# Performance work log

Measured on AMD Instinct MI355X. Metric: run time of the kernel, lower is better.

The kernel has to match this reference:

```python
import jax, jax.numpy as jnp
import numpy as np

VOCAB, NUM_CLASSES, E, H = 50257, 20, 64, 64
B, T = 128, 2048


def setup_inputs() -> dict:
    key = jax.random.key(0)
    ks = jax.random.split(key, 16)
    s_ih = 1.0 / np.sqrt(H)
    u = lambda k, shape: jax.random.uniform(k, shape, jnp.float32, -s_ih, s_ih)
    return {
        'tokens': jax.random.randint(ks[0], (B, T), 0, VOCAB),
        'emb': jax.random.normal(ks[1], (VOCAB, E), jnp.float32),
        # forward-direction GRU params (PyTorch layout: [3H, *], gate order r,z,n)
        'wih_f': u(ks[2], (3 * H, E)), 'whh_f': u(ks[3], (3 * H, H)),
        'bih_f': u(ks[4], (3 * H,)), 'bhh_f': u(ks[5], (3 * H,)),
        # backward-direction GRU params
        'wih_b': u(ks[6], (3 * H, E)), 'whh_b': u(ks[7], (3 * H, H)),
        'bih_b': u(ks[8], (3 * H,)), 'bhh_b': u(ks[9], (3 * H,)),
        # classifier: Linear(4H -> H), GELU, Linear(H -> C)
        'w1': u(ks[10], (H, 4 * H)), 'b1': u(ks[11], (H,)),
        'w2': u(ks[12], (NUM_CLASSES, H)), 'b2': u(ks[13], (NUM_CLASSES,)),
    }


def _gru_dir(x, wih, whh, bih, bhh):
    # x: [B, T, E] -> outputs [B, T, H]; PyTorch GRU gate math, gates (r, z, n)
    xg = jnp.einsum('bte,ge->tbg', x, wih) + bih  # precompute input projections [T,B,3H]
    h0 = jnp.zeros((x.shape[0], H), x.dtype)

    def step(h, xg_t):
        hg = h @ whh.T + bhh
        xr, xz, xn = jnp.split(xg_t, 3, axis=-1)
        hr, hz, hn = jnp.split(hg, 3, axis=-1)
        r = jax.nn.sigmoid(xr + hr)
        z = jax.nn.sigmoid(xz + hz)
        n = jnp.tanh(xn + r * hn)
        h_new = (1.0 - z) * n + z * h
        return h_new, h_new

    _, hs = jax.lax.scan(step, h0, xg)  # hs: [T, B, H]
    return hs.transpose(1, 0, 2)


def reference(tokens, emb, wih_f, whh_f, bih_f, bhh_f,
              wih_b, whh_b, bih_b, bhh_b, w1, b1, w2, b2):
    x = emb[tokens]  # [B, T, E]
    h_fwd = _gru_dir(x, wih_f, whh_f, bih_f, bhh_f)
    h_bwd = _gru_dir(x[:, ::-1], wih_b, whh_b, bih_b, bhh_b)[:, ::-1]
    encoded = jnp.concatenate([h_fwd, h_bwd], axis=-1)  # [B, T, 2H]
    feats = jnp.concatenate([encoded.mean(axis=1), encoded.max(axis=1)], axis=-1)  # [B, 4H]
    hid = jax.nn.gelu(feats @ w1.T + b1, approximate=False)
    return hid @ w2.T + b2  # [B, C]
```

## Files before the change

### kernel.cpp

```cpp
#include <hip/hip_runtime.h>
#include <hip/hip_bf16.h>
#include <math.h>

#define VOCAB 50257
#define NCLS 20
#define EDIM 64
#define HDIM 64
#define BATCH 128
#define TLEN 2048

typedef float v2f __attribute__((ext_vector_type(2)));

__device__ float g_P[(size_t)2 * VOCAB * 192];
__device__ float g_feats[BATCH * 256];

__device__ __forceinline__ float fast_rcp(float x) { return __builtin_amdgcn_rcpf(x); }

__device__ __forceinline__ float fsigmoid(float x) {
    return fast_rcp(1.f + __expf(-x));
}
__device__ __forceinline__ float ftanh(float x) {
    float e = __expf(2.f * x);
    return 1.f - 2.f * fast_rcp(e + 1.f);
}

__global__ __launch_bounds__(384) void precompute_P(
    const float* __restrict__ emb,
    const float* __restrict__ wih_f, const float* __restrict__ bih_f,
    const float* __restrict__ wih_b, const float* __restrict__ bih_b)
{
    const int t = threadIdx.x;
    const int dir = t / 192;
    const int g = t % 192;
    const float* wih = dir ? wih_b : wih_f;
    const float* bih = dir ? bih_b : bih_f;

    float4 wq0, wq1, wq2, wq3, wq4, wq5, wq6, wq7;
    float4 wq8, wq9, wq10, wq11, wq12, wq13, wq14, wq15;
#define LDWQ(K) wq##K = *(const float4*)(wih + (size_t)g * 64 + 4 * K)
    LDWQ(0); LDWQ(1); LDWQ(2); LDWQ(3); LDWQ(4); LDWQ(5); LDWQ(6); LDWQ(7);
    LDWQ(8); LDWQ(9); LDWQ(10); LDWQ(11); LDWQ(12); LDWQ(13); LDWQ(14); LDWQ(15);
#undef LDWQ
    const float bias = bih[g];
    float* Pd = g_P + (size_t)dir * VOCAB * 192;

    for (int v = blockIdx.x * 2; v < VOCAB; v += gridDim.x * 2) {
        const int v1ok = (v + 1 < VOCAB);
        const float4* e0 = (const float4*)(emb + (size_t)v * 64);
        const float4* e1 = (const float4*)(emb + (size_t)(v1ok ? v + 1 : v) * 64);
        float a0 = bias, a1 = bias;
#define PFMA(K) do {                                   \
            float4 x = e0[K];                          \
            float4 y = e1[K];                          \
            a0 = fmaf(x.x, wq##K.x, a0);               \
            a1 = fmaf(y.x, wq##K.x, a1);               \
            a0 = fmaf(x.y, wq##K.y, a0);               \
            a1 = fmaf(y.y, wq##K.y, a1);               \
            a0 = fmaf(x.z, wq##K.z, a0);               \
            a1 = fmaf(y.z, wq##K.z, a1);               \
            a0 = fmaf(x.w, wq##K.w, a0);               \
            a1 = fmaf(y.w, wq##K.w, a1);               \
        } while (0)
        PFMA(0); PFMA(1); PFMA(2); PFMA(3); PFMA(4); PFMA(5); PFMA(6); PFMA(7);
        PFMA(8); PFMA(9); PFMA(10); PFMA(11); PFMA(12); PFMA(13); PFMA(14); PFMA(15);
#undef PFMA
        Pd[(size_t)v * 192 + g] = a0;
        if (v1ok) Pd[(size_t)(v + 1) * 192 + g] = a1;
    }
}

__global__ __launch_bounds__(768, 1) void gru_seq(
    const int* __restrict__ tokens,
    const float* __restrict__ whh_f, const float* __restrict__ bhh_f,
    const float* __restrict__ whh_b, const float* __restrict__ bhh_b)
{
    const int tid = threadIdx.x;
    const int gate = tid >> 8;
    const int j = tid & 255;
    const int u = j >> 2;
    const int c = j & 3;
    const int blk = blockIdx.x;
    const int b = blk >> 1;
    const int dir = blk & 1;
    const float* whh = dir ? whh_b : whh_f;
    const float* bhh = dir ? bhh_b : bhh_f;
    const float* Pd = g_P + (size_t)dir * VOCAB * 192 + gate * 64 + u;

    __shared__ __align__(16) float h_lds[64];
    __shared__ float r_lds[64];
    __shared__ float z_lds[64];
    __shared__ __align__(16) int tok_lds[TLEN];

    {
        const int4* src = (const int4*)(tokens + (size_t)b * TLEN);
        int4* dst = (int4*)tok_lds;
        for (int t = tid; t < TLEN / 4; t += 768) dst[t] = src[t];
    }

    v2f w0, w1, w2, w3, w4, w5, w6, w7;
    {
        const float4* p = (const float4*)(whh + (size_t)(gate * 64 + u) * 64 + c * 16);
        float4 q0 = p[0]; w0 = (v2f){q0.x, q0.y}; w1 = (v2f){q0.z, q0.w};
        float4 q1 = p[1]; w2 = (v2f){q1.x, q1.y}; w3 = (v2f){q1.z, q1.w};
        float4 q2 = p[2]; w4 = (v2f){q2.x, q2.y}; w5 = (v2f){q2.z, q2.w};
        float4 q3 = p[3]; w6 = (v2f){q3.x, q3.y}; w7 = (v2f){q3.z, q3.w};
    }
    const float bias = bhh[gate * 64 + u];

    if (tid < 64) h_lds[tid] = 0.f;
    float h = 0.f, sum = 0.f, mx = -INFINITY;
    __syncthreads();

    auto tok_at = [&](int s) -> int {
        int ss = s < TLEN ? s : TLEN - 1;
        return tok_lds[dir ? (TLEN - 1 - ss) : ss];
    };

    float x0, x1, x2, x3;
#define GRU_PRE(SL, D) \
    asm volatile("global_load_dword %0, %1, off" : "=v"(x##SL) : "v"(Pd + (size_t)tok_at(D) * 192))
    GRU_PRE(0, 0); GRU_PRE(1, 1); GRU_PRE(2, 2); GRU_PRE(3, 3);

#define GRU_STEP(SL, SB) do {                                                      \
        const int tN_ = tok_at((SB) + 4);    \
        const float4* hb_ = (const float4*)(h_lds + c * 16);                       \
        v2f a0 = {0.f, 0.f}, a1 = {0.f, 0.f};                                      \
        { float4 h4_ = hb_[0];                                                     \
          a0 = __builtin_elementwise_fma((v2f){h4_.x, h4_.y}, w0, a0);             \
          a1 = __builtin_elementwise_fma((v2f){h4_.z, h4_.w}, w1, a1); }           \
        { float4 h4_ = hb_[1];                                                     \
          a0 = __builtin_elementwise_fma((v2f){h4_.x, h4_.y}, w2, a0);             \
          a1 = __builtin_elementwise_fma((v2f){h4_.z, h4_.w}, w3, a1); }           \
        { float4 h4_ = hb_[2];                                                     \
          a0 = __builtin_elementwise_fma((v2f){h4_.x, h4_.y}, w4, a0);             \
          a1 = __builtin_elementwise_fma((v2f){h4_.z, h4_.w}, w5, a1); }           \
        { float4 h4_ = hb_[3];                                                     \
          a0 = __builtin_elementwise_fma((v2f){h4_.x, h4_.y}, w6, a0);             \
          a1 = __builtin_elementwise_fma((v2f){h4_.z, h4_.w}, w7, a1); }           \
        float p_ = (a0.x + a0.y) + (a1.x + a1.y);                                  \
        float t_ = p_ + __shfl_xor(p_, 1);               \
        float hg = t_ + __shfl_xor(t_, 2);                                         \
        if (gate != 2) {                                                           \
                    \
            asm volatile("s_waitcnt vmcnt(3)" : "+v"(x##SL));                      \
            float g_ = fsigmoid(x##SL + hg + bias);                                \
            if (c == 0) (gate == 0 ? r_lds : z_lds)[u] = g_;                       \
            asm volatile("global_load_dword %0, %1, off"                           \
                         : "=v"(x##SL) : "v"(Pd + (size_t)tN_ * 192));             \
        }                                                                          \
        asm volatile("s_waitcnt lgkmcnt(0)" ::: "memory");   \
        __builtin_amdgcn_s_barrier();                          \
        __builtin_amdgcn_sched_barrier(0);                                         \
        if (gate == 2) {                                                           \
            asm volatile("s_waitcnt vmcnt(3)" : "+v"(x##SL));                      \
            float r_ = r_lds[u];                                                   \
            float z_ = z_lds[u];                                                   \
            float n_ = ftanh(x##SL + r_ * (hg + bias));                            \
            h = fmaf(z_, h - n_, n_);                           \
            sum += h;                                                              \
            mx = fmaxf(mx, h);                                                     \
            if (c == 0) h_lds[u] = h;                                              \
            asm volatile("global_load_dword %0, %1, off"                           \
                         : "=v"(x##SL) : "v"(Pd + (size_t)tN_ * 192));             \
        }                                                                          \
        asm volatile("s_waitcnt lgkmcnt(0)" ::: "memory");    \
        __builtin_amdgcn_s_barrier();                            \
        __builtin_amdgcn_sched_barrier(0);                                         \
    } while (0)

    for (int s = 0; s < TLEN; s += 4) {
        GRU_STEP(0, s + 0);
        GRU_STEP(1, s + 1);
        GRU_STEP(2, s + 2);
        GRU_STEP(3, s + 3);
    }
    asm volatile("s_waitcnt vmcnt(0)" ::: "memory");

    if (gate == 2 && c == 0) {
        g_feats[b * 256 + dir * 64 + u] = sum * (1.f / TLEN);
        g_feats[b * 256 + 128 + dir * 64 + u] = mx;
    }
#undef GRU_PRE
#undef GRU_STEP
}

__global__ __launch_bounds__(64) void classifier(
    const float* __restrict__ w1, const float* __restrict__ b1,
    const float* __restrict__ w2, const float* __restrict__ b2,
    float* __restrict__ out)
{
    const int b = blockIdx.x;
    const int i = threadIdx.x;
    __shared__ float f[256];
    __shared__ float hid[64];
    for (int c = i; c < 256; c += 64) f[c] = g_feats[b * 256 + c];
    __syncthreads();

    float acc = b1[i];
    const float* wrow = w1 + (size_t)i * 256;
#pragma unroll 16
    for (int c = 0; c < 256; c++) acc = fmaf(f[c], wrow[c], acc);
    hid[i] = acc * 0.5f * (1.f + erff(acc * 0.70710678118654752f));
    __syncthreads();

    if (i < NCLS) {
        float o = b2[i];
        const float* w2r = w2 + (size_t)i * 64;
#pragma unroll
        for (int j = 0; j < 64; j++) o = fmaf(hid[j], w2r[j], o);
        out[b * NCLS + i] = o;
    }
}

extern "C" void kernel_launch(void* const* d_in, const int* in_sizes, int n_in,
                              void* d_out, int out_size, void* d_ws, size_t ws_size,
                              hipStream_t stream) {
    const int*   tokens = (const int*)  d_in[0];
    const float* emb    = (const float*)d_in[1];
    const float* wih_f  = (const float*)d_in[2];
    const float* whh_f  = (const float*)d_in[3];
    const float* bih_f  = (const float*)d_in[4];
    const float* bhh_f  = (const float*)d_in[5];
    const float* wih_b  = (const float*)d_in[6];
    const float* whh_b  = (const float*)d_in[7];
    const float* bih_b  = (const float*)d_in[8];
    const float* bhh_b  = (const float*)d_in[9];
    const float* w1     = (const float*)d_in[10];
    const float* b1     = (const float*)d_in[11];
    const float* w2     = (const float*)d_in[12];
    const float* b2     = (const float*)d_in[13];
    float* out = (float*)d_out;

    precompute_P<<<4096, 384, 0, stream>>>(emb, wih_f, bih_f, wih_b, bih_b);
    gru_seq<<<2 * BATCH, 768, 0, stream>>>(tokens, whh_f, bhh_f, whh_b, bhh_b);
    classifier<<<BATCH, 64, 0, stream>>>(w1, b1, w2, b2, out);
}
```

Before: 972.8 us.

## Drop second per-step barrier by computing the hidden update redundantly in every wave

Every wave now computes the n-gate and the hidden-state update for all 64 units, and each writes the same h values to LDS. The r, z and recurrent-n results are double-buffered by step parity, so each recurrence step needs one block barrier instead of two. The cost is extra per-step work: every wave issues a second gathered load of the n-gate input projection and redundantly evaluates tanh and the state update. The intent is to shorten the latency-bound serial chain of 2048 steps.

```diff
diff --git a/kernel.cpp b/kernel.cpp
--- a/kernel.cpp
+++ b/kernel.cpp
@@ -79,16 +79,20 @@
     const int j = tid & 255;
     const int u = j >> 2;
     const int c = j & 3;
+    const int lane = tid & 63;
     const int blk = blockIdx.x;
     const int b = blk >> 1;
     const int dir = blk & 1;
     const float* whh = dir ? whh_b : whh_f;
     const float* bhh = dir ? bhh_b : bhh_f;
-    const float* Pd = g_P + (size_t)dir * VOCAB * 192 + gate * 64 + u;
+    const float* Pbase = g_P + (size_t)dir * VOCAB * 192;
+    const float* Pg = Pbase + gate * 64 + u;
+    const float* Pn = Pbase + 128 + lane;
 
     __shared__ __align__(16) float h_lds[64];
-    __shared__ float r_lds[64];
-    __shared__ float z_lds[64];
+    __shared__ float r_lds[2][64];
+    __shared__ float z_lds[2][64];
+    __shared__ float hnb_lds[2][64];
     __shared__ __align__(16) int tok_lds[TLEN];
 
     {
@@ -116,13 +120,17 @@
         return tok_lds[dir ? (TLEN - 1 - ss) : ss];
     };
 
-    float x0, x1, x2, x3;
-#define GRU_PRE(SL, D) \
-    asm volatile("global_load_dword %0, %1, off" : "=v"(x##SL) : "v"(Pd + (size_t)tok_at(D) * 192))
+    float xg0, xg1, xg2, xg3, xn0, xn1, xn2, xn3;
+#define GRU_PRE(SL, D) do {                                                        \
+        const size_t o_ = (size_t)tok_at(D) * 192;                                 \
+        asm volatile("global_load_dword %0, %1, off" : "=v"(xg##SL) : "v"(Pg + o_)); \
+        asm volatile("global_load_dword %0, %1, off" : "=v"(xn##SL) : "v"(Pn + o_)); \
+    } while (0)
     GRU_PRE(0, 0); GRU_PRE(1, 1); GRU_PRE(2, 2); GRU_PRE(3, 3);
 
-#define GRU_STEP(SL, SB) do {                                                      \
-        const int tN_ = tok_at((SB) + 4);    \
+#define GRU_STEP(SL, SB, PAR) do {                                                 \
+        const int tN_ = tok_at((SB) + 4);                                          \
+          \
         const float4* hb_ = (const float4*)(h_lds + c * 16);                       \
         v2f a0 = {0.f, 0.f}, a1 = {0.f, 0.f};                                      \
         { float4 h4_ = hb_[0];                                                     \
@@ -138,47 +146,48 @@
           a0 = __builtin_elementwise_fma((v2f){h4_.x, h4_.y}, w6, a0);             \
           a1 = __builtin_elementwise_fma((v2f){h4_.z, h4_.w}, w7, a1); }           \
         float p_ = (a0.x + a0.y) + (a1.x + a1.y);                                  \
-        float t_ = p_ + __shfl_xor(p_, 1);               \
+        float t_ = p_ + __shfl_xor(p_, 1);                                         \
         float hg = t_ + __shfl_xor(t_, 2);                                         \
-        if (gate != 2) {                                                           \
-                    \
-            asm volatile("s_waitcnt vmcnt(3)" : "+v"(x##SL));                      \
-            float g_ = fsigmoid(x##SL + hg + bias);                                \
-            if (c == 0) (gate == 0 ? r_lds : z_lds)[u] = g_;                       \
-            asm volatile("global_load_dword %0, %1, off"                           \
-                         : "=v"(x##SL) : "v"(Pd + (size_t)tN_ * 192));             \
+             \
+        asm volatile("s_waitcnt vmcnt(6)" : "+v"(xg##SL), "+v"(xn##SL));           \
+        if (gate == 2) {                                                           \
+            if (c == 0) hnb_lds[PAR][u] = hg + bias;                               \
+        } else {                                                                   \
+            float g_ = fsigmoid(xg##SL + hg + bias);                               \
+            if (c == 0) { float* d_ = (gate == 0) ? r_lds[PAR] : z_lds[PAR];       \
+                          d_[u] = g_; }                                            \
         }                                                                          \
-        asm volatile("s_waitcnt lgkmcnt(0)" ::: "memory");   \
-        __builtin_amdgcn_s_barrier();                          \
-        __builtin_amdgcn_sched_barrier(0);                                         \
-        if (gate == 2) {                                                           \
-            asm volatile("s_waitcnt vmcnt(3)" : "+v"(x##SL));                      \
-            float r_ = r_lds[u];                                                   \
-            float z_ = z_lds[u];                                                   \
-            float n_ = ftanh(x##SL + r_ * (hg + bias));                            \
+        asm volatile("s_waitcnt lgkmcnt(0)" ::: "memory");                         \
+        __builtin_amdgcn_s_barrier();                    \
+        asm volatile("" ::: "memory");                                             \
+                   \
+        {                                                                          \
+            float r_ = r_lds[PAR][lane];                                           \
+            float z_ = z_lds[PAR][lane];                                           \
+            float hnb_ = hnb_lds[PAR][lane];                                       \
+            float n_ = ftanh(xn##SL + r_ * hnb_);                                  \
             h = fmaf(z_, h - n_, n_);                           \
             sum += h;                                                              \
             mx = fmaxf(mx, h);                                                     \
-            if (c == 0) h_lds[u] = h;                                              \
-            asm volatile("global_load_dword %0, %1, off"                           \
-                         : "=v"(x##SL) : "v"(Pd + (size_t)tN_ * 192));             \
+            h_lds[lane] = h;            \
         }                                                                          \
-        asm volatile("s_waitcnt lgkmcnt(0)" ::: "memory");    \
-        __builtin_amdgcn_s_barrier();                            \
-        __builtin_amdgcn_sched_barrier(0);                                         \
+                                  \
+        const size_t o_ = (size_t)tN_ * 192;                                       \
+        asm volatile("global_load_dword %0, %1, off" : "=v"(xg##SL) : "v"(Pg + o_)); \
+        asm volatile("global_load_dword %0, %1, off" : "=v"(xn##SL) : "v"(Pn + o_)); \
     } while (0)
 
     for (int s = 0; s < TLEN; s += 4) {
-        GRU_STEP(0, s + 0);
-        GRU_STEP(1, s + 1);
-        GRU_STEP(2, s + 2);
-        GRU_STEP(3, s + 3);
+        GRU_STEP(0, s + 0, 0);
+        GRU_STEP(1, s + 1, 1);
+        GRU_STEP(2, s + 2, 0);
+        GRU_STEP(3, s + 3, 1);
     }
     asm volatile("s_waitcnt vmcnt(0)" ::: "memory");
 
-    if (gate == 2 && c == 0) {
-        g_feats[b * 256 + dir * 64 + u] = sum * (1.f / TLEN);
-        g_feats[b * 256 + 128 + dir * 64 + u] = mx;
+    if (tid < 64) {
+        g_feats[b * 256 + dir * 64 + lane] = sum * (1.f / TLEN);
+        g_feats[b * 256 + 128 + dir * 64 + lane] = mx;
     }
 #undef GRU_PRE
 #undef GRU_STEP
```

After: 1.090 ms. +12.1%, slower.
